# Optimization experiments

Measured on AMD Instinct MI355X. Metric: run time of the kernel, lower is better.

## Reference

```python
import jax, jax.numpy as jnp
import numpy as np

H = 256      # hidden_size
NH = 4       # num_heads
HD = H // NH # head_dim
N_NODES = 2048
N_EDGES = 8192
EPS = 1e-5


def _layer_norm(x, g, b):
    mu = jnp.mean(x, axis=-1, keepdims=True)
    var = jnp.mean((x - mu) ** 2, axis=-1, keepdims=True)
    return (x - mu) * jax.lax.rsqrt(var + EPS) * g + b


def setup_inputs() -> dict:
    key = jax.random.key(0)
    ks = jax.random.split(key, 16)
    s = 1.0 / np.sqrt(H)
    inp = {
        "node_features": jax.random.normal(ks[0], (N_NODES, H), jnp.float32),
        "edge_features": jax.random.normal(ks[1], (N_EDGES, H), jnp.float32),
        "in_proj_w": jax.random.uniform(ks[2], (3 * H, H), jnp.float32, -s, s),
        "in_proj_b": jnp.zeros((3 * H,), jnp.float32),
        "out_proj_w": jax.random.uniform(ks[3], (H, H), jnp.float32, -s, s),
        "out_proj_b": jnp.zeros((H,), jnp.float32),
        "mlp_w1": jax.random.uniform(ks[4], (H, H), jnp.float32, -s, s),
        "mlp_b1": jnp.zeros((H,), jnp.float32),
        "mlp_w2": jax.random.uniform(ks[5], (H, H), jnp.float32, -s, s),
        "mlp_b2": jnp.zeros((H,), jnp.float32),
        "nu_w": jax.random.uniform(ks[6], (H, H), jnp.float32, -s, s),
        "nu_b": jnp.zeros((H,), jnp.float32),
        "ln1_g": jnp.ones((H,), jnp.float32),
        "ln1_b": jnp.zeros((H,), jnp.float32),
        "ln2_g": jnp.ones((H,), jnp.float32),
        "ln2_b": jnp.zeros((H,), jnp.float32),
        "edge_index": jax.random.randint(ks[7], (2, N_EDGES), 0, N_NODES, jnp.int32),
    }
    return inp


def reference(node_features, edge_features, in_proj_w, in_proj_b, out_proj_w, out_proj_b,
              mlp_w1, mlp_b1, mlp_w2, mlp_b2, nu_w, nu_b,
              ln1_g, ln1_b, ln2_g, ln2_b, edge_index):
    x = edge_features  # [E, H]; torch MHA with batch=1, seq=E
    qkv = x @ in_proj_w.T + in_proj_b            # [E, 3H]
    q, k, v = jnp.split(qkv, 3, axis=-1)
    q = q.reshape(N_EDGES, NH, HD)
    k = k.reshape(N_EDGES, NH, HD)
    v = v.reshape(N_EDGES, NH, HD)
    scores = jnp.einsum('qhd,khd->hqk', q, k) / np.sqrt(HD)  # [NH, E, E]
    attn = jax.nn.softmax(scores, axis=-1)
    ctx = jnp.einsum('hqk,khd->qhd', attn, v).reshape(N_EDGES, H)
    attended = ctx @ out_proj_w.T + out_proj_b

    e = _layer_norm(edge_features + attended, ln1_g, ln1_b)
    mlp = jax.nn.relu(e @ mlp_w1.T + mlp_b1) @ mlp_w2.T + mlp_b2
    e = _layer_norm(e + mlp, ln2_g, ln2_b)

    dst = edge_index[1]
    seg_sum = jax.ops.segment_sum(e, dst, num_segments=N_NODES)           # [N, H]
    cnt = jax.ops.segment_sum(jnp.ones((N_EDGES,), e.dtype), dst, num_segments=N_NODES)
    node_updates = seg_sum / jnp.maximum(cnt, 1.0)[:, None]               # scatter_mean
    n = node_features + jax.nn.relu(node_updates @ nu_w.T + nu_b)
    return (n, e)
```

## Files before the change

### kernel.cpp

```cpp
#include <hip/hip_runtime.h>

typedef __bf16 bf16_t;
typedef __bf16 bf16x8 __attribute__((ext_vector_type(8)));
typedef __bf16 bf16x4 __attribute__((ext_vector_type(4)));
typedef unsigned short u16x8 __attribute__((ext_vector_type(8)));
typedef unsigned int u32x4 __attribute__((ext_vector_type(4)));
typedef float f32x4 __attribute__((ext_vector_type(4)));
typedef float f32x16 __attribute__((ext_vector_type(16)));
typedef int i32x2 __attribute__((ext_vector_type(2)));

#define NE 8192
#define NN 2048
#define HH 256
#define NSPLIT 4
#define QSCALE 0.18033688011112042f

#if __has_builtin(__builtin_amdgcn_exp2f)
#define EXP2(x) __builtin_amdgcn_exp2f(x)
#else
#define EXP2(x) exp2f(x)
#endif

__device__ inline f32x4 mfma16(bf16x8 a, bf16x8 b, f32x4 c) {
    return __builtin_amdgcn_mfma_f32_16x16x32_bf16(a, b, c, 0, 0, 0);
}
__device__ inline f32x16 mfma32(bf16x8 a, bf16x8 b, f32x16 c) {
    return __builtin_amdgcn_mfma_f32_32x32x16_bf16(a, b, c, 0, 0, 0);
}
__device__ inline unsigned cvtpk(float lo, float hi) {
    unsigned r;
    asm("v_cvt_pk_bf16_f32 %0, %1, %2" : "=v"(r) : "v"(lo), "v"(hi));
    return r;
}

__device__ inline bf16x4 cvt4(float4 v) {
    bf16x4 o;
    o[0] = (bf16_t)v.x; o[1] = (bf16_t)v.y; o[2] = (bf16_t)v.z; o[3] = (bf16_t)v.w;
    return o;
}

__global__ __launch_bounds__(256)
void convert_kernel(const float* __restrict__ ef, const float* __restrict__ wq,
                    const float* __restrict__ wo, const float* __restrict__ w1,
                    const float* __restrict__ w2, const float* __restrict__ wn,
                    bf16_t* __restrict__ ebf, bf16_t* __restrict__ bwq,
                    bf16_t* __restrict__ bwo, bf16_t* __restrict__ bw1,
                    bf16_t* __restrict__ bw2, bf16_t* __restrict__ bwn) {
    int i = blockIdx.x * 256 + threadIdx.x;
    ((bf16x4*)ebf)[i] = cvt4(((const float4*)ef)[i]);
    if (i < 49152) ((bf16x4*)bwq)[i] = cvt4(((const float4*)wq)[i]);
    if (i < 16384) {
        ((bf16x4*)bwo)[i] = cvt4(((const float4*)wo)[i]);
        ((bf16x4*)bw1)[i] = cvt4(((const float4*)w1)[i]);
        ((bf16x4*)bw2)[i] = cvt4(((const float4*)w2)[i]);
        ((bf16x4*)bwn)[i] = cvt4(((const float4*)wn)[i]);
    }
}

template<int ACT, int OUTKIND, int QSC = 0>
__global__ __launch_bounds__(256)
void gemm_kernel(const bf16_t* __restrict__ A, const bf16_t* __restrict__ B,
                 const float* __restrict__ bias, void* __restrict__ out,
                 const float* __restrict__ resid, int M, int N, int K) {
    __shared__ bf16_t As[64][72];
    __shared__ bf16_t Bs[64][72];
    int tid = threadIdx.x;
    int w = tid >> 6, l = tid & 63, hi = l >> 4, c15 = l & 15;
    int wr = w >> 1, wc = w & 1;
    int brow = blockIdx.x * 64, bcol = blockIdx.y * 64;
    int r = tid >> 2, s = tid & 3;

    f32x4 acc[2][2] = {};

    for (int k0 = 0; k0 < K; k0 += 64) {
        __syncthreads();
        bf16x8 a0 = *(const bf16x8*)&A[(long)(brow + r) * K + k0 + s * 16];
        bf16x8 a1 = *(const bf16x8*)&A[(long)(brow + r) * K + k0 + s * 16 + 8];
        bf16x8 b0 = *(const bf16x8*)&B[(long)(bcol + r) * K + k0 + s * 16];
        bf16x8 b1 = *(const bf16x8*)&B[(long)(bcol + r) * K + k0 + s * 16 + 8];
        *(bf16x8*)&As[r][s * 16]     = a0;
        *(bf16x8*)&As[r][s * 16 + 8] = a1;
        *(bf16x8*)&Bs[r][s * 16]     = b0;
        *(bf16x8*)&Bs[r][s * 16 + 8] = b1;
        __syncthreads();
#pragma unroll
        for (int c = 0; c < 2; ++c) {
            bf16x8 af0 = *(const bf16x8*)&As[wr * 32 + c15][c * 32 + hi * 8];
            bf16x8 af1 = *(const bf16x8*)&As[wr * 32 + 16 + c15][c * 32 + hi * 8];
            bf16x8 bf0 = *(const bf16x8*)&Bs[wc * 32 + c15][c * 32 + hi * 8];
            bf16x8 bf1 = *(const bf16x8*)&Bs[wc * 32 + 16 + c15][c * 32 + hi * 8];
            acc[0][0] = mfma16(af0, bf0, acc[0][0]);
            acc[0][1] = mfma16(af0, bf1, acc[0][1]);
            acc[1][0] = mfma16(af1, bf0, acc[1][0]);
            acc[1][1] = mfma16(af1, bf1, acc[1][1]);
        }
    }

    float sc = (QSC && bcol < 256) ? QSCALE : 1.0f;
#pragma unroll
    for (int i = 0; i < 2; ++i)
#pragma unroll
        for (int j = 0; j < 2; ++j)
#pragma unroll
            for (int rg = 0; rg < 4; ++rg) {
                int row = brow + wr * 32 + i * 16 + hi * 4 + rg;
                int col = bcol + wc * 32 + j * 16 + c15;
                float v = (acc[i][j][rg] + bias[col]) * sc;
                if (ACT) v = fmaxf(v, 0.0f);
                if (OUTKIND == 0) {
                    ((float*)out)[(long)row * N + col] = v;
                } else if (OUTKIND == 1) {
                    ((bf16_t*)out)[(long)row * N + col] = (bf16_t)v;
                } else {
                    ((float*)out)[(long)row * N + col] =
                        resid[(long)row * N + col] + fmaxf(v, 0.0f);
                }
            }
}

__global__ __launch_bounds__(256, 2)
void attn_kernel(const bf16_t* __restrict__ qkv, float* __restrict__ Opart,
                 float* __restrict__ lpart) {
    __shared__ char smem[36864];
    bf16_t (*Ks)[64][72] = (bf16_t (*)[64][72])smem;
    bf16_t (*Vt)[64][72] = (bf16_t (*)[64][72])(smem + 18432);

    int h = blockIdx.x & 3, qb = blockIdx.x >> 2, sp = blockIdx.y;
    int q0 = qb * 256;
    int tid = threadIdx.x;
    int wv = tid >> 6, l = tid & 63, l31 = l & 31, h8 = l >> 5;

    bf16x8 qf[2][4];
#pragma unroll
    for (int qt = 0; qt < 2; ++qt)
#pragma unroll
        for (int dc = 0; dc < 4; ++dc)
            qf[qt][dc] = *(const bf16x8*)&qkv[
                (size_t)(q0 + wv * 64 + qt * 32 + l31) * 768 + h * 64 + dc * 16 + h8 * 8];

    f32x16 o[2][2];
#pragma unroll
    for (int a = 0; a < 2; ++a)
#pragma unroll
        for (int b = 0; b < 2; ++b)
#pragma unroll
            for (int r = 0; r < 16; ++r) o[a][b][r] = 0.f;
    float ls[2] = {0.f, 0.f};

    int kr = tid >> 2, ksc = tid & 3;
    int vp = tid & 31, vc = tid >> 5;
    int kv0 = sp * (NE / NSPLIT);
    const int NT = (NE / NSPLIT) / 64;

    bf16x8 kst0, kst1, vst0, vst1;
    {
        const bf16_t* ksrc = &qkv[(size_t)(kv0 + kr) * 768 + 256 + h * 64 + ksc * 16];
        kst0 = *(const bf16x8*)ksrc; kst1 = *(const bf16x8*)(ksrc + 8);
        const bf16_t* vsrc = &qkv[(size_t)(kv0 + 2 * vp) * 768 + 512 + h * 64 + vc * 8];
        vst0 = *(const bf16x8*)vsrc; vst1 = *(const bf16x8*)(vsrc + 768);
    }
    {
        *(bf16x8*)&Ks[0][kr][ksc * 16]     = kst0;
        *(bf16x8*)&Ks[0][kr][ksc * 16 + 8] = kst1;
        u16x8 ua = __builtin_bit_cast(u16x8, vst0), ub = __builtin_bit_cast(u16x8, vst1);
#pragma unroll
        for (int j = 0; j < 8; ++j) {
            unsigned wd = (unsigned)ua[j] | ((unsigned)ub[j] << 16);
            *(unsigned*)&Vt[0][vc * 8 + j][2 * vp] = wd;
        }
    }

    for (int t = 0; t < NT; ++t) {
        int cur = t & 1;
        __syncthreads();
        if (t + 1 < NT) {
            int kt = kv0 + (t + 1) * 64;
            const bf16_t* ksrc = &qkv[(size_t)(kt + kr) * 768 + 256 + h * 64 + ksc * 16];
            kst0 = *(const bf16x8*)ksrc; kst1 = *(const bf16x8*)(ksrc + 8);
            const bf16_t* vsrc = &qkv[(size_t)(kt + 2 * vp) * 768 + 512 + h * 64 + vc * 8];
            vst0 = *(const bf16x8*)vsrc; vst1 = *(const bf16x8*)(vsrc + 768);
        }

#pragma unroll
        for (int kvt = 0; kvt < 2; ++kvt) {
            bf16x8 kf[4];
#pragma unroll
            for (int dc = 0; dc < 4; ++dc)
                kf[dc] = *(const bf16x8*)&Ks[cur][kvt * 32 + l31][dc * 16 + h8 * 8];
            f32x16 s[2];
#pragma unroll
            for (int qt = 0; qt < 2; ++qt) {
#pragma unroll
                for (int r = 0; r < 16; ++r) s[qt][r] = 0.f;
#pragma unroll
                for (int dc = 0; dc < 4; ++dc)
                    s[qt] = mfma32(kf[dc], qf[qt][dc], s[qt]);
            }
            bf16x8 bfr[2][2];
#pragma unroll
            for (int qt = 0; qt < 2; ++qt) {
                float p[16];
#pragma unroll
                for (int r = 0; r < 16; ++r) { p[r] = EXP2(s[qt][r]); ls[qt] += p[r]; }
#pragma unroll
                for (int half = 0; half < 2; ++half) {
                    i32x2 r0 = __builtin_amdgcn_permlane32_swap(
                        (int)cvtpk(p[8 * half + 0], p[8 * half + 1]),
                        (int)cvtpk(p[8 * half + 4], p[8 * half + 5]), false, false);
                    i32x2 r1 = __builtin_amdgcn_permlane32_swap(
                        (int)cvtpk(p[8 * half + 2], p[8 * half + 3]),
                        (int)cvtpk(p[8 * half + 6], p[8 * half + 7]), false, false);
                    u32x4 wds;
                    wds[0] = (unsigned)r0[0]; wds[1] = (unsigned)r1[0];
                    wds[2] = (unsigned)r0[1]; wds[3] = (unsigned)r1[1];
                    bfr[qt][half] = __builtin_bit_cast(bf16x8, wds);
                }
            }
#pragma unroll
            for (int dt = 0; dt < 2; ++dt) {
                bf16x8 vf[2];
#pragma unroll
                for (int half = 0; half < 2; ++half)
                    vf[half] = *(const bf16x8*)&Vt[cur][dt * 32 + l31][(kvt * 2 + half) * 16 + h8 * 8];
#pragma unroll
                for (int qt = 0; qt < 2; ++qt)
#pragma unroll
                    for (int half = 0; half < 2; ++half)
                        o[dt][qt] = mfma32(vf[half], bfr[qt][half], o[dt][qt]);
            }
        }

        if (t + 1 < NT) {
            int nb = (t + 1) & 1;
            *(bf16x8*)&Ks[nb][kr][ksc * 16]     = kst0;
            *(bf16x8*)&Ks[nb][kr][ksc * 16 + 8] = kst1;
            u16x8 ua = __builtin_bit_cast(u16x8, vst0), ub = __builtin_bit_cast(u16x8, vst1);
#pragma unroll
            for (int j = 0; j < 8; ++j) {
                unsigned wd = (unsigned)ua[j] | ((unsigned)ub[j] << 16);
                *(unsigned*)&Vt[nb][vc * 8 + j][2 * vp] = wd;
            }
        }
    }

#pragma unroll
    for (int qt = 0; qt < 2; ++qt) {
        float lt = ls[qt] + __shfl_xor(ls[qt], 32);
        if (l < 32)
            lpart[((size_t)sp * 4 + h) * NE + q0 + wv * 64 + qt * 32 + l31] = lt;
    }

    float* Of = (float*)smem;
#pragma unroll
    for (int pass = 0; pass < 2; ++pass) {
        __syncthreads();
        if ((wv >> 1) == pass) {
#pragma unroll
            for (int dt = 0; dt < 2; ++dt)
#pragma unroll
                for (int qt = 0; qt < 2; ++qt)
#pragma unroll
                    for (int r = 0; r < 16; ++r) {
                        int qrel = (wv & 1) * 64 + qt * 32 + l31;
                        int d = dt * 32 + (r & 3) + 8 * (r >> 2) + 4 * h8;
                        Of[qrel * 68 + d] = o[dt][qt][r];
                    }
        }
        __syncthreads();
        {
            int rr = tid >> 1, hf = tid & 1;
            float* dst = &Opart[(size_t)sp * NE * 256 +
                                (size_t)(q0 + pass * 128 + rr) * 256 + h * 64 + hf * 32];
#pragma unroll
            for (int i = 0; i < 8; ++i) {
                float4 v = *(float4*)&Of[rr * 68 + hf * 32 + i * 4];
                *(float4*)&dst[i * 4] = v;
            }
        }
    }
}

__global__ __launch_bounds__(256)
void attn_merge_kernel(const float* __restrict__ Opart, const float* __restrict__ lpart,
                       bf16_t* __restrict__ ctx) {
    int i = blockIdx.x * 256 + threadIdx.x;
    int q = i >> 6, c4 = i & 63, h = c4 >> 4;
    float4 sum = {0.f, 0.f, 0.f, 0.f};
    float lsum = 0.f;
#pragma unroll
    for (int sp = 0; sp < NSPLIT; ++sp) {
        float4 v = ((const float4*)Opart)[(size_t)sp * (NE * 64) + i];
        sum.x += v.x; sum.y += v.y; sum.z += v.z; sum.w += v.w;
        lsum += lpart[((size_t)sp * 4 + h) * NE + q];
    }
    float rl = 1.0f / lsum;
    bf16x4 c;
    c[0] = (bf16_t)(sum.x * rl); c[1] = (bf16_t)(sum.y * rl);
    c[2] = (bf16_t)(sum.z * rl); c[3] = (bf16_t)(sum.w * rl);
    ((bf16x4*)ctx)[i] = c;
}

__global__ __launch_bounds__(256)
void ln_kernel(const float* __restrict__ x, const float* __restrict__ y,
               const float* __restrict__ g, const float* __restrict__ b,
               float* __restrict__ outf, bf16_t* __restrict__ outb) {
    int row = blockIdx.x * 4 + (threadIdx.x >> 6);
    int l = threadIdx.x & 63;
    float4 v = ((const float4*)&x[(long)row * 256])[l];
    float4 uu = ((const float4*)&y[(long)row * 256])[l];
    float a0 = v.x + uu.x, a1 = v.y + uu.y, a2 = v.z + uu.z, a3 = v.w + uu.w;

    float s = a0 + a1 + a2 + a3;
#pragma unroll
    for (int off = 1; off < 64; off <<= 1) s += __shfl_xor(s, off);
    float mu = s * (1.0f / 256.0f);

    float d0 = a0 - mu, d1 = a1 - mu, d2 = a2 - mu, d3 = a3 - mu;
    float q = d0 * d0 + d1 * d1 + d2 * d2 + d3 * d3;
#pragma unroll
    for (int off = 1; off < 64; off <<= 1) q += __shfl_xor(q, off);
    float rs = rsqrtf(q * (1.0f / 256.0f) + 1e-5f);

    float4 gg = ((const float4*)g)[l];
    float4 bb = ((const float4*)b)[l];
    float o0 = d0 * rs * gg.x + bb.x;
    float o1 = d1 * rs * gg.y + bb.y;
    float o2 = d2 * rs * gg.z + bb.z;
    float o3 = d3 * rs * gg.w + bb.w;
    float4 ov; ov.x = o0; ov.y = o1; ov.z = o2; ov.w = o3;
    ((float4*)&outf[(long)row * 256])[l] = ov;
    if (outb) {
        bf16x4 ob;
        ob[0] = (bf16_t)o0; ob[1] = (bf16_t)o1; ob[2] = (bf16_t)o2; ob[3] = (bf16_t)o3;
        ((bf16x4*)&outb[(long)row * 256])[l] = ob;
    }
}

__global__ __launch_bounds__(256)
void scatter_kernel(const float* __restrict__ e, const int* __restrict__ ei,
                    float* __restrict__ acc, float* __restrict__ cnt) {
    int edge = blockIdx.x;
    int dst = ei[NE + edge];
    int t = threadIdx.x;
    atomicAdd(&acc[(long)dst * 256 + t], e[(long)edge * 256 + t]);
    if (t == 0) atomicAdd(&cnt[dst], 1.0f);
}

__global__ __launch_bounds__(256)
void upd_kernel(const float* __restrict__ acc, const float* __restrict__ cnt,
                bf16_t* __restrict__ ub) {
    int i = blockIdx.x * 256 + threadIdx.x;
    int row = i >> 8;
    ub[i] = (bf16_t)(acc[i] / fmaxf(cnt[row], 1.0f));
}

extern "C" void kernel_launch(void* const* d_in, const int* in_sizes, int n_in,
                              void* d_out, int out_size, void* d_ws, size_t ws_size,
                              hipStream_t stream) {
    const float* node_features = (const float*)d_in[0];
    const float* edge_features = (const float*)d_in[1];
    const float* in_proj_w  = (const float*)d_in[2];
    const float* in_proj_b  = (const float*)d_in[3];
    const float* out_proj_w = (const float*)d_in[4];
    const float* out_proj_b = (const float*)d_in[5];
    const float* mlp_w1 = (const float*)d_in[6];
    const float* mlp_b1 = (const float*)d_in[7];
    const float* mlp_w2 = (const float*)d_in[8];
    const float* mlp_b2 = (const float*)d_in[9];
    const float* nu_w   = (const float*)d_in[10];
    const float* nu_b   = (const float*)d_in[11];
    const float* ln1_g  = (const float*)d_in[12];
    const float* ln1_b  = (const float*)d_in[13];
    const float* ln2_g  = (const float*)d_in[14];
    const float* ln2_b  = (const float*)d_in[15];
    const int*   edge_index = (const int*)d_in[16];

    char* ws = (char*)d_ws;
    size_t off = 0;
    auto alloc = [&](size_t bytes) {
        char* p = ws + off;
        off = (off + bytes + 255) & ~(size_t)255;
        return p;
    };
    bf16_t* ebf   = (bf16_t*)alloc(NE * HH * 2);
    bf16_t* bwq   = (bf16_t*)alloc(768 * 256 * 2);
    bf16_t* bwo   = (bf16_t*)alloc(256 * 256 * 2);
    bf16_t* bw1   = (bf16_t*)alloc(256 * 256 * 2);
    bf16_t* bw2   = (bf16_t*)alloc(256 * 256 * 2);
    bf16_t* bwn   = (bf16_t*)alloc(256 * 256 * 2);
    bf16_t* qkv   = (bf16_t*)alloc((size_t)NE * 768 * 2);
    bf16_t* ctx   = (bf16_t*)alloc((size_t)NE * HH * 2);
    float*  lpart = (float*)alloc((size_t)NSPLIT * 4 * NE * 4);
    float*  acc   = (float*)alloc((size_t)(NN * HH + NN) * 4);
    float*  cnt   = acc + (size_t)NN * HH;
    bf16_t* updb  = (bf16_t*)alloc((size_t)NN * HH * 2);
    size_t offB = off;
    float*  Opart = (float*)alloc((size_t)NSPLIT * NE * HH * 4);
    off = offB;
    float*  attended = (float*)alloc((size_t)NE * HH * 4);
    float*  e1f   = (float*)alloc((size_t)NE * HH * 4);
    bf16_t* e1b   = (bf16_t*)alloc((size_t)NE * HH * 2);
    bf16_t* hbuf  = (bf16_t*)alloc((size_t)NE * HH * 2);
    float*  mlpout = (float*)alloc((size_t)NE * HH * 4);

    float* nout = (float*)d_out;
    float* eout = (float*)d_out + (size_t)NN * HH;

    convert_kernel<<<2048, 256, 0, stream>>>(edge_features, in_proj_w, out_proj_w,
                                             mlp_w1, mlp_w2, nu_w,
                                             ebf, bwq, bwo, bw1, bw2, bwn);

    gemm_kernel<0, 1, 1><<<dim3(NE / 64, 768 / 64), 256, 0, stream>>>(
        ebf, bwq, in_proj_b, qkv, nullptr, NE, 768, 256);

    attn_kernel<<<dim3(128, NSPLIT), 256, 0, stream>>>(qkv, Opart, lpart);
    attn_merge_kernel<<<2048, 256, 0, stream>>>(Opart, lpart, ctx);

    gemm_kernel<0, 0><<<dim3(NE / 64, 256 / 64), 256, 0, stream>>>(
        ctx, bwo, out_proj_b, attended, nullptr, NE, 256, 256);

    ln_kernel<<<NE / 4, 256, 0, stream>>>(edge_features, attended, ln1_g, ln1_b,
                                          e1f, e1b);

    gemm_kernel<1, 1><<<dim3(NE / 64, 256 / 64), 256, 0, stream>>>(
        e1b, bw1, mlp_b1, hbuf, nullptr, NE, 256, 256);

    gemm_kernel<0, 0><<<dim3(NE / 64, 256 / 64), 256, 0, stream>>>(
        hbuf, bw2, mlp_b2, mlpout, nullptr, NE, 256, 256);

    ln_kernel<<<NE / 4, 256, 0, stream>>>(e1f, mlpout, ln2_g, ln2_b,
                                          eout, (bf16_t*)nullptr);

    hipMemsetAsync(acc, 0, (size_t)(NN * HH + NN) * 4, stream);
    scatter_kernel<<<NE, 256, 0, stream>>>(eout, edge_index, acc, cnt);
    upd_kernel<<<NN * HH / 256, 256, 0, stream>>>(acc, cnt, updb);

    gemm_kernel<0, 2><<<dim3(NN / 64, 256 / 64), 256, 0, stream>>>(
        updb, bwn, nu_b, nout, node_features, NN, 256, 256);
}
```

Baseline: 147.6 us.

## Double attention KV splits, store partial outputs in bf16, raise occupancy hint

Raises the flash-attention key split count from 4 to 8, giving 1024 blocks instead of 512 to fill more of the GPU. Partial outputs are now written in bf16 instead of fp32, so the larger split count does not double partial-buffer traffic. The merge kernel is vectorised to handle 8 bf16 values per thread, and the attention kernel's launch bound asks for 4 blocks per CU. The cost is extra bf16 rounding of unnormalised partial sums, more merge work, and register pressure from the higher occupancy target, which could cause spills.

```diff
diff --git a/kernel.cpp b/kernel.cpp
--- a/kernel.cpp
+++ b/kernel.cpp
@@ -12,7 +12,7 @@
 #define NE 8192
 #define NN 2048
 #define HH 256
-#define NSPLIT 4
+#define NSPLIT 8
 #define QSCALE 0.18033688011112042f
 
 #if __has_builtin(__builtin_amdgcn_exp2f)
@@ -118,8 +118,8 @@
             }
 }
 
-__global__ __launch_bounds__(256, 2)
-void attn_kernel(const bf16_t* __restrict__ qkv, float* __restrict__ Opart,
+__global__ __launch_bounds__(256, 4)
+void attn_kernel(const bf16_t* __restrict__ qkv, bf16_t* __restrict__ Opart,
                  float* __restrict__ lpart) {
     __shared__ char smem[36864];
     bf16_t (*Ks)[64][72] = (bf16_t (*)[64][72])smem;
@@ -269,35 +269,43 @@
         __syncthreads();
         {
             int rr = tid >> 1, hf = tid & 1;
-            float* dst = &Opart[(size_t)sp * NE * 256 +
-                                (size_t)(q0 + pass * 128 + rr) * 256 + h * 64 + hf * 32];
-#pragma unroll
-            for (int i = 0; i < 8; ++i) {
-                float4 v = *(float4*)&Of[rr * 68 + hf * 32 + i * 4];
-                *(float4*)&dst[i * 4] = v;
-            }
-        }
-    }
-}
-
-__global__ __launch_bounds__(256)
-void attn_merge_kernel(const float* __restrict__ Opart, const float* __restrict__ lpart,
+            bf16_t* dst = &Opart[(size_t)sp * NE * 256 +
+                                 (size_t)(q0 + pass * 128 + rr) * 256 + h * 64 + hf * 32];
+#pragma unroll
+            for (int i = 0; i < 4; ++i) {
+                float4 va = *(float4*)&Of[rr * 68 + hf * 32 + i * 8];
+                float4 vb = *(float4*)&Of[rr * 68 + hf * 32 + i * 8 + 4];
+                bf16x8 ob;
+                ob[0] = (bf16_t)va.x; ob[1] = (bf16_t)va.y;
+                ob[2] = (bf16_t)va.z; ob[3] = (bf16_t)va.w;
+                ob[4] = (bf16_t)vb.x; ob[5] = (bf16_t)vb.y;
+                ob[6] = (bf16_t)vb.z; ob[7] = (bf16_t)vb.w;
+                *(bf16x8*)&dst[i * 8] = ob;
+            }
+        }
+    }
+}
+
+__global__ __launch_bounds__(256)
+void attn_merge_kernel(const bf16_t* __restrict__ Opart, const float* __restrict__ lpart,
                        bf16_t* __restrict__ ctx) {
     int i = blockIdx.x * 256 + threadIdx.x;
-    int q = i >> 6, c4 = i & 63, h = c4 >> 4;
-    float4 sum = {0.f, 0.f, 0.f, 0.f};
+    int q = i >> 5;
+    int h = (i & 31) >> 3;
+    float sum[8] = {};
     float lsum = 0.f;
 #pragma unroll
     for (int sp = 0; sp < NSPLIT; ++sp) {
-        float4 v = ((const float4*)Opart)[(size_t)sp * (NE * 64) + i];
-        sum.x += v.x; sum.y += v.y; sum.z += v.z; sum.w += v.w;
+        bf16x8 v = ((const bf16x8*)Opart)[(size_t)sp * (NE * 32) + i];
+#pragma unroll
+        for (int j = 0; j < 8; ++j) sum[j] += (float)v[j];
         lsum += lpart[((size_t)sp * 4 + h) * NE + q];
     }
     float rl = 1.0f / lsum;
-    bf16x4 c;
-    c[0] = (bf16_t)(sum.x * rl); c[1] = (bf16_t)(sum.y * rl);
-    c[2] = (bf16_t)(sum.z * rl); c[3] = (bf16_t)(sum.w * rl);
-    ((bf16x4*)ctx)[i] = c;
+    bf16x8 c;
+#pragma unroll
+    for (int j = 0; j < 8; ++j) c[j] = (bf16_t)(sum[j] * rl);
+    ((bf16x8*)ctx)[i] = c;
 }
 
 __global__ __launch_bounds__(256)
@@ -395,7 +403,7 @@
     float*  cnt   = acc + (size_t)NN * HH;
     bf16_t* updb  = (bf16_t*)alloc((size_t)NN * HH * 2);
     size_t offB = off;
-    float*  Opart = (float*)alloc((size_t)NSPLIT * NE * HH * 4);
+    bf16_t* Opart = (bf16_t*)alloc((size_t)NSPLIT * NE * HH * 2);
     off = offB;
     float*  attended = (float*)alloc((size_t)NE * HH * 4);
     float*  e1f   = (float*)alloc((size_t)NE * HH * 4);
@@ -414,7 +422,7 @@
         ebf, bwq, in_proj_b, qkv, nullptr, NE, 768, 256);
 
     attn_kernel<<<dim3(128, NSPLIT), 256, 0, stream>>>(qkv, Opart, lpart);
-    attn_merge_kernel<<<2048, 256, 0, stream>>>(Opart, lpart, ctx);
+    attn_merge_kernel<<<1024, 256, 0, stream>>>(Opart, lpart, ctx);
 
     gemm_kernel<0, 0><<<dim3(NE / 64, 256 / 64), 256, 0, stream>>>(
         ctx, bwo, out_proj_b, attended, nullptr, NE, 256, 256);
```

Result: slower. 406.2 us (+175.1%).
